# Kernel tuning notes

Hardware: AMD Instinct MI355X
Metric: run time of the kernel (lower is better)

## Reference

```python
import jax, jax.numpy as jnp
import numpy as np

B, C, O, K, H, W, CH = 32, 256, 256, 3, 56, 56, 4  # batch, in_planes, out_planes, kernel, spatial, in_chunk
STRIDE, PAD, DIL = 1, 1, 1


def setup_inputs() -> dict:
    key = jax.random.key(0)
    ks = jax.random.split(key, 5)
    gain = np.sqrt(2.0).astype(np.float32)  # calculate_gain('relu')
    x = jax.random.normal(ks[0], (B, C, H, W), jnp.float32)
    # CWFF: fc1 1x1 conv (C->C, no bias), fc2 1x1 conv (C->CH*C, bias)
    fc1_w = jax.random.normal(ks[1], (C, C), jnp.float32) * np.sqrt(2.0 / C).astype(np.float32)  # kaiming fan_out
    fc2_w = jax.random.normal(ks[2], (CH * C, C), jnp.float32) * np.sqrt(2.0 / (CH * C)).astype(np.float32)
    fc2_b = jnp.zeros((CH * C,), jnp.float32)
    cog_weight = jax.random.normal(ks[3], (O, CH, K, K), jnp.float32) * (gain * (CH * K * K) ** -0.5)
    weight = jax.random.normal(ks[4], (O, C, K, K), jnp.float32) * (gain * (C * K * K) ** -0.5)
    return dict(x=x, fc1_w=fc1_w, fc2_w=fc2_w, fc2_b=fc2_b, cog_weight=cog_weight, weight=weight)


def reference(x, fc1_w, fc2_w, fc2_b, cog_weight, weight):
    # CWFF: global avg pool -> 1x1 conv -> relu -> 1x1 conv
    pooled = x.mean(axis=(2, 3))                       # [B, C]
    h = jax.nn.relu(pooled @ fc1_w.T)                  # [B, C]
    kern = h @ fc2_w.T + fc2_b                         # [B, CH*C]
    # torch view(-1, in_chunk, 1, 1): channel dim splits as (c, ch)
    kern = kern.reshape(B, C, CH)                      # [B, C, CH]
    # cognitive weights: conv2d(cog_weight, kernel) == contraction over in_chunk
    cw = jnp.einsum('bct,otij->bocij', kern, cog_weight)   # [B, O, C, K, K]
    dyn_w = jax.nn.sigmoid(cw) * weight[None]               # per-sample kernels [B, O, C, K, K]
    # per-sample conv (groups=B in the original grouped-conv trick)
    def conv1(xi, wi):
        return jax.lax.conv_general_dilated(
            xi[None], wi,
            window_strides=(STRIDE, STRIDE),
            padding=[(PAD, PAD), (PAD, PAD)],
            rhs_dilation=(DIL, DIL))[0]
    return jax.vmap(conv1)(x, dyn_w)                   # [B, O, H, W]
```

## Files before the change

kernel.cpp:

```cpp
#include <hip/hip_runtime.h>

typedef unsigned short u16;
typedef __attribute__((ext_vector_type(4))) float f32x4;
typedef __attribute__((ext_vector_type(8))) short s16x8;
typedef __attribute__((ext_vector_type(4))) unsigned short u16x4;

static __device__ __forceinline__ u16 f2bf(float f) {
    unsigned int x = __float_as_uint(f);
    x += 0x7fffu + ((x >> 16) & 1u);
    return (u16)(x >> 16);
}

__global__ __launch_bounds__(256) void pool_kernel(const float* __restrict__ x,
                                                   float* __restrict__ pooled) {
    int bc = blockIdx.x;
    const float* p = x + (size_t)bc * 3136;
    float s = 0.f;
    for (int i = threadIdx.x; i < 784; i += 256) {
        f32x4 v = *(const f32x4*)(p + i * 4);
        s += v.x + v.y + v.z + v.w;
    }
#pragma unroll
    for (int off = 32; off; off >>= 1) s += __shfl_xor(s, off);
    __shared__ float red[4];
    int lane = threadIdx.x & 63, wave = threadIdx.x >> 6;
    if (lane == 0) red[wave] = s;
    __syncthreads();
    if (threadIdx.x == 0)
        pooled[bc] = (red[0] + red[1] + red[2] + red[3]) * (1.0f / 3136.0f);
}

__global__ __launch_bounds__(256) void fc1_kernel(const float* __restrict__ pooled,
                                                  const float* __restrict__ w,
                                                  float* __restrict__ h) {
    __shared__ float pv[256];
    int b = blockIdx.x >> 6;
    pv[threadIdx.x] = pooled[b * 256 + threadIdx.x];
    __syncthreads();
    int lane = threadIdx.x & 63, wave = threadIdx.x >> 6;
    int i = ((blockIdx.x & 63) << 2) + wave;
    f32x4 v = *(const f32x4*)(w + i * 256 + lane * 4);
    float s = v.x * pv[lane * 4 + 0] + v.y * pv[lane * 4 + 1] +
              v.z * pv[lane * 4 + 2] + v.w * pv[lane * 4 + 3];
#pragma unroll
    for (int off = 32; off; off >>= 1) s += __shfl_xor(s, off);
    if (lane == 0) h[b * 256 + i] = fmaxf(s, 0.f);
}

__global__ __launch_bounds__(256) void fc2_kernel(const float* __restrict__ h,
                                                  const float* __restrict__ w,
                                                  const float* __restrict__ bias,
                                                  float* __restrict__ kern) {
    __shared__ float hv[256];
    int b = blockIdx.x >> 8;
    hv[threadIdx.x] = h[b * 256 + threadIdx.x];
    __syncthreads();
    int lane = threadIdx.x & 63, wave = threadIdx.x >> 6;
    int i = ((blockIdx.x & 255) << 2) + wave;
    f32x4 v = *(const f32x4*)(w + i * 256 + lane * 4);
    float s = v.x * hv[lane * 4 + 0] + v.y * hv[lane * 4 + 1] +
              v.z * hv[lane * 4 + 2] + v.w * hv[lane * 4 + 3];
#pragma unroll
    for (int off = 32; off; off >>= 1) s += __shfl_xor(s, off);
    if (lane == 0) kern[b * 1024 + i] = s + bias[i];
}

__global__ __launch_bounds__(256) void dynw_kernel(const float* __restrict__ kern,
                                                   const float* __restrict__ cogw,
                                                   const float* __restrict__ wgt,
                                                   u16* __restrict__ dynw) {
    int idx = blockIdx.x * 256 + threadIdx.x;
    int cg = idx & 63;
    int p  = (idx >> 6) % 9;
    int bo = idx / 576;
    int o  = bo & 255;
    int b  = idx / 147456;
    const float* kp = kern + b * 1024 + cg * 16;
    float c0 = cogw[(o * 4 + 0) * 9 + p];
    float c1 = cogw[(o * 4 + 1) * 9 + p];
    float c2 = cogw[(o * 4 + 2) * 9 + p];
    float c3 = cogw[(o * 4 + 3) * 9 + p];
    u16x4 outv;
#pragma unroll
    for (int i = 0; i < 4; ++i) {
        f32x4 k4 = *(const f32x4*)(kp + i * 4);
        float cw = k4.x * c0 + k4.y * c1 + k4.z * c2 + k4.w * c3;
        float sg = 1.0f / (1.0f + __expf(-cw));
        float wv = wgt[(o * 256 + cg * 4 + i) * 9 + p];
        outv[i] = f2bf(sg * wv);
    }
    *(u16x4*)(dynw + ((size_t)bo * 9 + p) * 256 + cg * 4) = outv;
}

#define LDSW 40
__global__ __launch_bounds__(256, 2) void conv_kernel(const float* __restrict__ x,
                                                      const u16* __restrict__ dynw,
                                                      float* __restrict__ out) {
    __shared__ u16 lds[4 * 58 * LDSW];
    const int tid = threadIdx.x;
    const int wave = tid >> 6, lane = tid & 63;
    const int l15 = lane & 15, quad = lane >> 4;
    const int gid = blockIdx.x;
    const int slot = gid >> 3;
    const int b = (gid & 7) * 4 + slot / 28;
    const int stile = slot % 28;
    const int y0 = stile * 2;

    for (int i = tid; i < 320; i += 256) {
        int side = i & 1, j = i >> 1;
        int yy = j / LDSW, c = j % LDSW;
        lds[(yy * 58 + (side ? 57 : 0)) * LDSW + c] = 0;
    }

    f32x4 acc[4][7];
#pragma unroll
    for (int mf = 0; mf < 4; ++mf)
#pragma unroll
        for (int nf = 0; nf < 7; ++nf) acc[mf][nf] = (f32x4){0.f, 0.f, 0.f, 0.f};

    int bbase[7];
#pragma unroll
    for (int nf = 0; nf < 7; ++nf) {
        int n = nf * 16 + l15;
        int r = (n >= 56) ? 1 : 0;
        int xx = n - 56 * r;
        bbase[nf] = (r * 58 + xx) * LDSW + quad * 8;
    }
    const u16* Abase = dynw + ((size_t)b * 256 + wave * 64 + l15) * 2304 + quad * 8;
    const float* Xb = x + (size_t)b * 256 * 3136;

    __syncthreads();
    for (int cc = 0; cc < 8; ++cc) {
#pragma unroll
        for (int it = 0; it < 7; ++it) {
            int i = it * 256 + tid;
            int c = i / 56, rem = i % 56;
            int yy = rem / 14, xg = rem % 14;
            int yg = y0 - 1 + yy;
            f32x4 v = (f32x4){0.f, 0.f, 0.f, 0.f};
            if ((unsigned)yg < 56u)
                v = *(const f32x4*)(Xb + ((size_t)(cc * 32 + c) * 56 + yg) * 56 + xg * 4);
            int base = (yy * 58 + 1 + xg * 4) * LDSW + c;
            lds[base]            = f2bf(v.x);
            lds[base + LDSW]     = f2bf(v.y);
            lds[base + 2 * LDSW] = f2bf(v.z);
            lds[base + 3 * LDSW] = f2bf(v.w);
        }
        __syncthreads();
#pragma unroll
        for (int p = 0; p < 9; ++p) {
            const int dy = p / 3, dx = p % 3;
            const int tapoff = (dy * 58 + dx) * LDSW;
            s16x8 a0 = *(const s16x8*)(Abase + 0 * 36864 + p * 256 + cc * 32);
            s16x8 a1 = *(const s16x8*)(Abase + 1 * 36864 + p * 256 + cc * 32);
            s16x8 a2 = *(const s16x8*)(Abase + 2 * 36864 + p * 256 + cc * 32);
            s16x8 a3 = *(const s16x8*)(Abase + 3 * 36864 + p * 256 + cc * 32);
#pragma unroll
            for (int nf = 0; nf < 7; ++nf) {
                s16x8 bf = *(const s16x8*)(&lds[bbase[nf] + tapoff]);
                acc[0][nf] = __builtin_amdgcn_mfma_f32_16x16x32_bf16(a0, bf, acc[0][nf], 0, 0, 0);
                acc[1][nf] = __builtin_amdgcn_mfma_f32_16x16x32_bf16(a1, bf, acc[1][nf], 0, 0, 0);
                acc[2][nf] = __builtin_amdgcn_mfma_f32_16x16x32_bf16(a2, bf, acc[2][nf], 0, 0, 0);
                acc[3][nf] = __builtin_amdgcn_mfma_f32_16x16x32_bf16(a3, bf, acc[3][nf], 0, 0, 0);
            }
        }
        __syncthreads();
    }
#pragma unroll
    for (int mf = 0; mf < 4; ++mf) {
        int o = wave * 64 + mf * 16 + quad * 4;
        size_t obase = ((size_t)b * 256 + o) * 3136 + (size_t)stile * 112 + l15;
#pragma unroll
        for (int nf = 0; nf < 7; ++nf) {
#pragma unroll
            for (int r = 0; r < 4; ++r)
                out[obase + (size_t)r * 3136 + nf * 16] = acc[mf][nf][r];
        }
    }
}

extern "C" void kernel_launch(void* const* d_in, const int* in_sizes, int n_in,
                              void* d_out, int out_size, void* d_ws, size_t ws_size,
                              hipStream_t stream) {
    const float* x    = (const float*)d_in[0];
    const float* fc1w = (const float*)d_in[1];
    const float* fc2w = (const float*)d_in[2];
    const float* fc2b = (const float*)d_in[3];
    const float* cogw = (const float*)d_in[4];
    const float* wgt  = (const float*)d_in[5];
    float* out = (float*)d_out;

    char* ws = (char*)d_ws;
    float* pooled = (float*)ws;
    float* h      = (float*)(ws + 32768);
    float* kern   = (float*)(ws + 65536);
    u16*   dynw   = (u16*)(ws + 196608);

    pool_kernel<<<8192, 256, 0, stream>>>(x, pooled);
    fc1_kernel<<<2048, 256, 0, stream>>>(pooled, fc1w, h);
    fc2_kernel<<<8192, 256, 0, stream>>>(h, fc2w, fc2b, kern);
    dynw_kernel<<<18432, 256, 0, stream>>>(kern, cogw, wgt, dynw);
    conv_kernel<<<896, 256, 0, stream>>>(x, dynw, out);
}
```

Baseline: 394.9 us.

## Restructure dynamic-weight generation and vectorize conv input staging to LDS

The dynamic-weight kernel now gives each block one output channel and eight batches. It stages that channel's base weights in shared memory, keeps cognitive weights in registers and reuses them across batches, which replaces 18432 blocks with scattered loads by 1024 blocks. The conv kernel's input staging now has each thread read four channels at one pixel and write a packed 4-element bf16 vector to LDS, instead of four scalar LDS stores per float4 load. Padding zeroing also uses vector stores. Global reads of x become per-channel scalar strided loads rather than float4 loads, which may reduce load efficiency, and dynw stores are now 2-byte scalar writes.

After: 384.6 us. -2.6%, faster.

```diff
diff --git a/kernel.cpp b/kernel.cpp
--- a/kernel.cpp
+++ b/kernel.cpp
@@ -69,27 +69,38 @@
                                                    const float* __restrict__ cogw,
                                                    const float* __restrict__ wgt,
                                                    u16* __restrict__ dynw) {
-    int idx = blockIdx.x * 256 + threadIdx.x;
-    int cg = idx & 63;
-    int p  = (idx >> 6) % 9;
-    int bo = idx / 576;
-    int o  = bo & 255;
-    int b  = idx / 147456;
-    const float* kp = kern + b * 1024 + cg * 16;
-    float c0 = cogw[(o * 4 + 0) * 9 + p];
-    float c1 = cogw[(o * 4 + 1) * 9 + p];
-    float c2 = cogw[(o * 4 + 2) * 9 + p];
-    float c3 = cogw[(o * 4 + 3) * 9 + p];
-    u16x4 outv;
-#pragma unroll
-    for (int i = 0; i < 4; ++i) {
-        f32x4 k4 = *(const f32x4*)(kp + i * 4);
-        float cw = k4.x * c0 + k4.y * c1 + k4.z * c2 + k4.w * c3;
-        float sg = 1.0f / (1.0f + __expf(-cw));
-        float wv = wgt[(o * 256 + cg * 4 + i) * 9 + p];
-        outv[i] = f2bf(sg * wv);
-    }
-    *(u16x4*)(dynw + ((size_t)bo * 9 + p) * 256 + cg * 4) = outv;
+    __shared__ float wl[2304];
+    const int o = blockIdx.x & 255;
+    const int bg = blockIdx.x >> 8;
+    const int c = threadIdx.x;
+    const float* wo = wgt + (size_t)o * 2304;
+#pragma unroll
+    for (int j = 0; j < 9; ++j)
+        wl[j * 256 + c] = wo[j * 256 + c];
+    __syncthreads();
+
+    float cg0[9], cg1[9], cg2[9], cg3[9];
+#pragma unroll
+    for (int p = 0; p < 9; ++p) {
+        cg0[p] = cogw[(o * 4 + 0) * 9 + p];
+        cg1[p] = cogw[(o * 4 + 1) * 9 + p];
+        cg2[p] = cogw[(o * 4 + 2) * 9 + p];
+        cg3[p] = cogw[(o * 4 + 3) * 9 + p];
+    }
+    float w9[9];
+#pragma unroll
+    for (int p = 0; p < 9; ++p) w9[p] = wl[c * 9 + p];
+
+    for (int b = bg * 8; b < bg * 8 + 8; ++b) {
+        f32x4 k4 = *(const f32x4*)(kern + b * 1024 + c * 4);
+        u16* dst = dynw + (size_t)(b * 256 + o) * 9 * 256 + c;
+#pragma unroll
+        for (int p = 0; p < 9; ++p) {
+            float cw = k4.x * cg0[p] + k4.y * cg1[p] + k4.z * cg2[p] + k4.w * cg3[p];
+            float sg = 1.0f / (1.0f + __expf(-cw));
+            dst[p * 256] = f2bf(sg * w9[p]);
+        }
+    }
 }
 
 #define LDSW 40
@@ -106,10 +117,9 @@
     const int stile = slot % 28;
     const int y0 = stile * 2;
 
-    for (int i = tid; i < 320; i += 256) {
-        int side = i & 1, j = i >> 1;
-        int yy = j / LDSW, c = j % LDSW;
-        lds[(yy * 58 + (side ? 57 : 0)) * LDSW + c] = 0;
+    if (tid < 64) {
+        int side = tid & 1, yy = (tid >> 1) & 3, cg = tid >> 3;
+        *(u16x4*)&lds[(yy * 58 + (side ? 57 : 0)) * LDSW + cg * 4] = (u16x4){0, 0, 0, 0};
     }
 
     f32x4 acc[4][7];
@@ -134,17 +144,20 @@
 #pragma unroll
         for (int it = 0; it < 7; ++it) {
             int i = it * 256 + tid;
-            int c = i / 56, rem = i % 56;
-            int yy = rem / 14, xg = rem % 14;
+            int q = i / 56;
+            int xx = i - q * 56;
+            int yy = q & 3;
+            int cg = q >> 2;
             int yg = y0 - 1 + yy;
-            f32x4 v = (f32x4){0.f, 0.f, 0.f, 0.f};
-            if ((unsigned)yg < 56u)
-                v = *(const f32x4*)(Xb + ((size_t)(cc * 32 + c) * 56 + yg) * 56 + xg * 4);
-            int base = (yy * 58 + 1 + xg * 4) * LDSW + c;
-            lds[base]            = f2bf(v.x);
-            lds[base + LDSW]     = f2bf(v.y);
-            lds[base + 2 * LDSW] = f2bf(v.z);
-            lds[base + 3 * LDSW] = f2bf(v.w);
+            u16x4 w = (u16x4){0, 0, 0, 0};
+            if ((unsigned)yg < 56u) {
+                const float* src = Xb + (size_t)(cc * 32 + cg * 4) * 3136 + yg * 56 + xx;
+                w.x = f2bf(src[0]);
+                w.y = f2bf(src[3136]);
+                w.z = f2bf(src[2 * 3136]);
+                w.w = f2bf(src[3 * 3136]);
+            }
+            *(u16x4*)&lds[(yy * 58 + 1 + xx) * LDSW + cg * 4] = w;
         }
         __syncthreads();
 #pragma unroll
@@ -199,6 +212,6 @@
     pool_kernel<<<8192, 256, 0, stream>>>(x, pooled);
     fc1_kernel<<<2048, 256, 0, stream>>>(pooled, fc1w, h);
     fc2_kernel<<<8192, 256, 0, stream>>>(h, fc2w, fc2b, kern);
-    dynw_kernel<<<18432, 256, 0, stream>>>(kern, cogw, wgt, dynw);
+    dynw_kernel<<<1024, 256, 0, stream>>>(kern, cogw, wgt, dynw);
     conv_kernel<<<896, 256, 0, stream>>>(x, dynw, out);
 }
```
